# Kernel optimization log

Hardware: AMD Instinct MI355X
Metric: run time of the kernel (lower is better)

Reference implementation:

```python
import jax, jax.numpy as jnp
import numpy as np

EMBED_DIM = 768
N_HEADS = 12
HEAD_SIZE = EMBED_DIM // N_HEADS


def setup_inputs() -> dict:
    key = jax.random.key(0)
    k1, k2, k3, k4 = jax.random.split(key, 4)
    B, T, C = 512, 128, EMBED_DIM
    x = jax.random.normal(k1, (B, T, C), dtype=jnp.float32)
    # torch Linear weights: [out, in]
    w_qkv = jax.random.normal(k2, (3 * C, C), dtype=jnp.float32) / np.sqrt(C)
    w_proj = jax.random.normal(k3, (C, C), dtype=jnp.float32) / np.sqrt(C)
    b_proj = jax.random.normal(k4, (C,), dtype=jnp.float32) * 0.01
    return {"x": x, "w_qkv": w_qkv, "w_proj": w_proj, "b_proj": b_proj}


def reference(x, w_qkv, w_proj, b_proj):
    B, T, C = x.shape
    H, D = N_HEADS, HEAD_SIZE
    qkv = jnp.einsum('btc,oc->bto', x, w_qkv)  # [B,T,3C]
    q, k, v = jnp.split(qkv, 3, axis=-1)
    # [B,T,C] -> [B,H,T,D]
    q = q.reshape(B, T, H, D).transpose(0, 2, 1, 3)
    k = k.reshape(B, T, H, D).transpose(0, 2, 1, 3)
    v = v.reshape(B, T, H, D).transpose(0, 2, 1, 3)
    wei = jnp.einsum('bhtd,bhsd->bhts', q, k)  # [B,H,T,T]
    causal = jnp.tril(jnp.ones((T, T), dtype=bool))  # True where allowed
    wei = jnp.where(causal, wei, -jnp.inf)
    # original scales AFTER masking (-inf stays -inf)
    wei = jax.nn.softmax(wei / jnp.sqrt(jnp.asarray(D, x.dtype)), axis=-1)
    out = jnp.einsum('bhts,bhsd->bhtd', wei, v)  # [B,H,T,D]
    out = out.transpose(0, 2, 1, 3).reshape(B, T, C)
    # proj; dropout is identity in eval mode
    out = jnp.einsum('btc,oc->bto', out, w_proj) + b_proj
    return out
```

## Files before the change

### kernel.cpp

```cpp
#include <hip/hip_runtime.h>
#include <hip/hip_bf16.h>

typedef __bf16 bf16_t;
typedef __attribute__((ext_vector_type(8))) __bf16 bf16x8;
typedef __attribute__((ext_vector_type(4))) float f32x4;

#define B_SZ 512
#define T_SZ 128
#define C_SZ 768
#define H_SZ 12
#define D_SZ 64
#define M_SZ (B_SZ * T_SZ)
#define NQKV (3 * C_SZ)

__device__ __forceinline__ void cvt8(const float* in, bf16_t* out)
{
    float4 a = *reinterpret_cast<const float4*>(in);
    float4 b = *reinterpret_cast<const float4*>(in + 4);
    bf16x8 o;
    o[0] = (bf16_t)a.x; o[1] = (bf16_t)a.y;
    o[2] = (bf16_t)a.z; o[3] = (bf16_t)a.w;
    o[4] = (bf16_t)b.x; o[5] = (bf16_t)b.y;
    o[6] = (bf16_t)b.z; o[7] = (bf16_t)b.w;
    *reinterpret_cast<bf16x8*>(out) = o;
}

__global__ __launch_bounds__(256) void cvt3_f32_bf16(
    const float* __restrict__ x,  bf16_t* __restrict__ xb,
    const float* __restrict__ wq, bf16_t* __restrict__ wqb,
    const float* __restrict__ wp, bf16_t* __restrict__ wpb,
    int nx, int nq, int np)
{
    const int tot = (nx + nq + np) >> 3;
    int c = blockIdx.x * blockDim.x + threadIdx.x;
    const int stride = gridDim.x * blockDim.x;
    for (; c < tot; c += stride) {
        int i = c << 3;
        if (i < nx)            cvt8(x + i, xb + i);
        else if (i < nx + nq)  cvt8(wq + (i - nx), wqb + (i - nx));
        else                   cvt8(wp + (i - nx - nq), wpb + (i - nx - nq));
    }
}

__device__ __forceinline__ void gload16(const bf16_t* g, const char* l)
{
    __builtin_amdgcn_global_load_lds(
        (const __attribute__((address_space(1))) void*)g,
        (__attribute__((address_space(3))) void*)l, 16, 0, 0);
}

#define BAR() do { asm volatile("" ::: "memory"); \
                   __builtin_amdgcn_s_barrier(); \
                   asm volatile("" ::: "memory"); } while (0)

#define VMC(n) asm volatile("s_waitcnt vmcnt(" #n ")" ::: "memory")

#define LGKM0() do { asm volatile("s_waitcnt lgkmcnt(0)" ::: "memory"); \
                     __builtin_amdgcn_sched_barrier(0); } while (0)

#define RD_A0(bb) do { _Pragma("unroll") for (int m_ = 0; m_ < 4; ++m_) { \
    af0[m_][0] = *(const bf16x8*)(rdAk0 + (bb)*32768 + m_*2048); \
    af0[m_][1] = *(const bf16x8*)(rdAk1 + (bb)*32768 + m_*2048); } } while (0)

#define RD_AY(bb) do { _Pragma("unroll") for (int m_ = 0; m_ < 4; ++m_) { \
    afY[m_][0] = *(const bf16x8*)(rdAk0 + (bb)*32768 + 8192 + m_*2048); \
    afY[m_][1] = *(const bf16x8*)(rdAk1 + (bb)*32768 + 8192 + m_*2048); } } while (0)

#define RD_B01(bb) do { _Pragma("unroll") for (int n_ = 0; n_ < 2; ++n_) { \
    b01[n_][0] = *(const bf16x8*)(rdBk0 + (bb)*32768 + n_*2048); \
    b01[n_][1] = *(const bf16x8*)(rdBk1 + (bb)*32768 + n_*2048); } } while (0)

#define RD_B23(bb) do { _Pragma("unroll") for (int n_ = 0; n_ < 2; ++n_) { \
    b23[n_][0] = *(const bf16x8*)(rdBk0 + (bb)*32768 + 4096 + n_*2048); \
    b23[n_][1] = *(const bf16x8*)(rdBk1 + (bb)*32768 + 4096 + n_*2048); } } while (0)

#define ST_A(bb, hf, u) do { if ((u) < nt) { \
    const bf16_t* s_ = pA + (size_t)((hf)*128) * K + (size_t)(u)*64; \
    char* d_ = ldsAw + (bb)*32768 + (hf)*16384; \
    gload16(s_, d_); gload16(s_ + (size_t)8*K, d_ + 1024); } } while (0)

#define ST_B(bb, hf, u) do { if ((u) < nt) { \
    const bf16_t* s_ = pB + (size_t)((hf)*128) * K + (size_t)(u)*64; \
    char* d_ = ldsBw + (bb)*32768 + (hf)*16384; \
    gload16(s_, d_); gload16(s_ + (size_t)8*K, d_ + 1024); } } while (0)

#define MFQ(A_, B_, mo, no) do { \
    _Pragma("unroll") for (int m_ = 0; m_ < 4; ++m_) \
    _Pragma("unroll") for (int n_ = 0; n_ < 2; ++n_) { \
        acc[(mo)+m_][(no)+n_] = __builtin_amdgcn_mfma_f32_16x16x32_bf16( \
            A_[m_][0], B_[n_][0], acc[(mo)+m_][(no)+n_], 0, 0, 0); \
        acc[(mo)+m_][(no)+n_] = __builtin_amdgcn_mfma_f32_16x16x32_bf16( \
            A_[m_][1], B_[n_][1], acc[(mo)+m_][(no)+n_], 0, 0, 0); } \
    } while (0)

template <bool BF16_OUT, bool BIAS>
__global__ __launch_bounds__(512, 2) void gemm256(
    const bf16_t* __restrict__ A, const bf16_t* __restrict__ Bt,
    void* __restrict__ Cout, const float* __restrict__ bias,
    int M, int N, int K, int nx)
{
    __shared__ char smem[131072];

    const int tid  = threadIdx.x;
    const int lane = tid & 63;
    const int w    = tid >> 6;
    const int wr   = w >> 2;
    const int wc   = w & 3;

    const int nwg = gridDim.x;
    int bid = blockIdx.x;
    if ((nwg & 7) == 0) bid = (bid & 7) * (nwg >> 3) + (bid >> 3);
    const int bx = bid % nx;
    const int by = bid / nx;
    const size_t bm = (size_t)by * 256;
    const size_t bn = (size_t)bx * 256;

    const int nt    = K >> 6;
    const int niter = nt >> 1;

    const int i3    = lane >> 3;
    const int colSw = ((lane & 7) ^ i3) * 8;
    const bf16_t* pA = A  + (bm + (size_t)(w * 16 + i3)) * K + colSw;
    const bf16_t* pB = Bt + (bn + (size_t)(w * 16 + i3)) * K + colSw;
    char* ldsAw = smem + w * 2048;
    char* ldsBw = smem + 65536 + w * 2048;

    const int lane_lo = lane & 15;
    const int sxr  = (lane & 7) << 4;
    const int cK0  = (((lane >> 4) * 16) ^ sxr);
    const int cK1  = cK0 ^ 64;
    const char* rdAk0 = smem + wr * 16384 + lane_lo * 128 + cK0;
    const char* rdAk1 = smem + wr * 16384 + lane_lo * 128 + cK1;
    const char* rdBk0 = smem + 65536 + (wc >> 1) * 16384 + ((wc & 1) * 64 + lane_lo) * 128 + cK0;
    const char* rdBk1 = smem + 65536 + (wc >> 1) * 16384 + ((wc & 1) * 64 + lane_lo) * 128 + cK1;

    f32x4  acc[8][4] = {};
    bf16x8 af0[4][2], afY[4][2], b01[2][2], b23[2][2];

    ST_B(0, 0, 0); ST_A(0, 0, 0); ST_A(0, 1, 0); ST_B(0, 1, 0);
    ST_B(1, 0, 1); ST_A(1, 0, 1);
    VMC(4);
    BAR();

    for (int it = 0; it < niter; ++it) {
        const int u = it * 2;
        const bool last = (it + 1 == niter);
        RD_A0(0); RD_B01(0); RD_B23(0); ST_A(1, 1, u + 1); MFQ(af0, b01, 0, 0); BAR();
        RD_AY(0);                        ST_B(1, 1, u + 1); MFQ(af0, b23, 0, 2); BAR();
                                         ST_B(0, 0, u + 2); MFQ(afY, b01, 4, 0); BAR();
                                         ST_A(0, 0, u + 2); MFQ(afY, b23, 4, 2);
        if (last) { VMC(0); } else { VMC(4); }
        BAR();
        RD_A0(1); RD_B01(1); RD_B23(1); ST_A(0, 1, u + 2); MFQ(af0, b01, 0, 0); BAR();
        RD_AY(1);                        ST_B(0, 1, u + 2); MFQ(af0, b23, 0, 2); BAR();
                                         ST_B(1, 0, u + 3); MFQ(afY, b01, 4, 0); BAR();
                                         ST_A(1, 0, u + 3); MFQ(afY, b23, 4, 2);
        if (last) { VMC(0); } else { VMC(4); }
        BAR();
    }

    const int crow = (lane >> 4) * 4;
    const int ccol = lane & 15;
    if constexpr (BF16_OUT) {
        char* ep = smem + w * 16384;
        #pragma unroll
        for (int n = 0; n < 4; ++n) {
            const size_t col = bn + wc * 64 + n * 16 + ccol;
            float bv = 0.f;
            if constexpr (BIAS) bv = bias[col];
            #pragma unroll
            for (int m = 0; m < 8; ++m)
                #pragma unroll
                for (int r = 0; r < 4; ++r) {
                    const int rowloc = m * 16 + crow + r;
                    const int sw = ((rowloc & 7) << 4) ^ (((rowloc >> 3) & 1) << 5);
                    *(bf16_t*)(ep + rowloc * 128 + (((n * 16 + ccol) * 2) ^ sw))
                        = (bf16_t)(acc[m][n][r] + bv);
                }
        }
        LGKM0();
        bf16_t* cb = (bf16_t*)Cout;
        #pragma unroll
        for (int pass = 0; pass < 16; ++pass) {
            const int rloc = pass * 8 + (lane >> 3);
            const int ch   = lane & 7;
            const int sw   = ((rloc & 7) << 4) ^ (((rloc >> 3) & 1) << 5);
            bf16x8 v = *(const bf16x8*)(ep + rloc * 128 + ((ch * 16) ^ sw));
            *(bf16x8*)((char*)(cb + (bm + wr * 128 + rloc) * (size_t)N + bn + wc * 64) + ch * 16) = v;
        }
    } else {
        #pragma unroll
        for (int n = 0; n < 4; ++n) {
            const size_t col = bn + wc * 64 + n * 16 + ccol;
            float bv = 0.f;
            if constexpr (BIAS) bv = bias[col];
            #pragma unroll
            for (int m = 0; m < 8; ++m) {
                #pragma unroll
                for (int r = 0; r < 4; ++r) {
                    const size_t row = bm + wr * 128 + m * 16 + crow + r;
                    ((float*)Cout)[row * N + col] = acc[m][n][r] + bv;
                }
            }
        }
    }
}

__global__ __launch_bounds__(256) void attn_kernel(
    const bf16_t* __restrict__ qkv, bf16_t* __restrict__ outp)
{
    __shared__ bf16_t Ks[128 * 64];
    __shared__ bf16_t Vt[64 * 128];
    __shared__ bf16_t Ps[128 * 128];

    const int h    = blockIdx.x;
    const int b    = blockIdx.y;
    const int tid  = threadIdx.x;
    const int lane = tid & 63;
    const int wave = tid >> 6;

    const bf16_t* base = qkv + (size_t)b * T_SZ * NQKV + h * D_SZ;

    bf16x8 qf[2][2];
    #pragma unroll
    for (int mi = 0; mi < 2; ++mi)
        #pragma unroll
        for (int ks = 0; ks < 2; ++ks) {
            int m = wave * 32 + mi * 16 + (lane & 15);
            int d = ks * 32 + (lane >> 4) * 8;
            qf[mi][ks] = *reinterpret_cast<const bf16x8*>(base + (size_t)m * NQKV + d);
        }

    #pragma unroll
    for (int p = 0; p < 4; ++p) {
        int e   = p * 256 + tid;
        int row = e >> 3;
        int col = (e & 7) * 8;
        int4 kv = *reinterpret_cast<const int4*>(base + (size_t)row * NQKV + C_SZ + col);
        int kb = row * 128 + ((col * 2) ^ ((row & 7) << 4));
        *reinterpret_cast<int4*>((char*)Ks + kb) = kv;

        bf16x8 vv = *reinterpret_cast<const bf16x8*>(base + (size_t)row * NQKV + 2 * C_SZ + col);
        #pragma unroll
        for (int j = 0; j < 8; ++j) {
            int d  = col + j;
            int vb = d * 256 + ((row * 2) ^ ((d & 7) << 4));
            *reinterpret_cast<bf16_t*>((char*)Vt + vb) = vv[j];
        }
    }

    __syncthreads();

    f32x4 s[2][8] = {};
    #pragma unroll
    for (int ks = 0; ks < 2; ++ks) {
        int koff = ks * 32 + (lane >> 4) * 8;
        #pragma unroll
        for (int nj = 0; nj < 8; ++nj) {
            int n  = nj * 16 + (lane & 15);
            int kb = n * 128 + ((koff * 2) ^ ((n & 7) << 4));
            bf16x8 kf = *reinterpret_cast<const bf16x8*>((char*)Ks + kb);
            #pragma unroll
            for (int mi = 0; mi < 2; ++mi)
                s[mi][nj] = __builtin_amdgcn_mfma_f32_16x16x32_bf16(
                    qf[mi][ks], kf, s[mi][nj], 0, 0, 0);
        }
    }

    const float scale = 0.125f;
    #pragma unroll
    for (int mi = 0; mi < 2; ++mi) {
        #pragma unroll
        for (int r = 0; r < 4; ++r) {
            int m = wave * 32 + mi * 16 + ((lane >> 4) << 2) + r;
            float sv[8];
            float mx = -3.0e38f;
            #pragma unroll
            for (int nj = 0; nj < 8; ++nj) {
                int n   = nj * 16 + (lane & 15);
                float v = s[mi][nj][r] * scale;
                v = (n <= m) ? v : -3.0e38f;
                sv[nj] = v;
                mx = fmaxf(mx, v);
            }
            #pragma unroll
            for (int off = 1; off < 16; off <<= 1)
                mx = fmaxf(mx, __shfl_xor(mx, off));
            float sum = 0.f;
            #pragma unroll
            for (int nj = 0; nj < 8; ++nj) {
                float p = __expf(sv[nj] - mx);
                sv[nj] = p;
                sum += p;
            }
            #pragma unroll
            for (int off = 1; off < 16; off <<= 1)
                sum += __shfl_xor(sum, off);
            float inv = 1.0f / sum;
            #pragma unroll
            for (int nj = 0; nj < 8; ++nj) {
                int n  = nj * 16 + (lane & 15);
                int pb = m * 256 + ((n * 2) ^ ((m & 7) << 4));
                *reinterpret_cast<bf16_t*>((char*)Ps + pb) = (bf16_t)(sv[nj] * inv);
            }
        }
    }

    __syncthreads();

    f32x4 o[2][4] = {};
    #pragma unroll
    for (int ks = 0; ks < 4; ++ks) {
        int soff = ks * 32 + (lane >> 4) * 8;
        bf16x8 pf[2];
        #pragma unroll
        for (int mi = 0; mi < 2; ++mi) {
            int m  = wave * 32 + mi * 16 + (lane & 15);
            int pb = m * 256 + ((soff * 2) ^ ((m & 7) << 4));
            pf[mi] = *reinterpret_cast<const bf16x8*>((char*)Ps + pb);
        }
        #pragma unroll
        for (int nj = 0; nj < 4; ++nj) {
            int d  = nj * 16 + (lane & 15);
            int vb = d * 256 + ((soff * 2) ^ ((d & 7) << 4));
            bf16x8 vf = *reinterpret_cast<const bf16x8*>((char*)Vt + vb);
            #pragma unroll
            for (int mi = 0; mi < 2; ++mi)
                o[mi][nj] = __builtin_amdgcn_mfma_f32_16x16x32_bf16(
                    pf[mi], vf, o[mi][nj], 0, 0, 0);
        }
    }

    char* on = (char*)Ks;
    #pragma unroll
    for (int mi = 0; mi < 2; ++mi)
        #pragma unroll
        for (int nj = 0; nj < 4; ++nj)
            #pragma unroll
            for (int r = 0; r < 4; ++r) {
                int m = wave * 32 + mi * 16 + ((lane >> 4) << 2) + r;
                int d = nj * 16 + (lane & 15);
                *(bf16_t*)(on + m * 128 + d * 2) = (bf16_t)o[mi][nj][r];
            }

    __syncthreads();

    bf16_t* op = outp + (size_t)b * T_SZ * C_SZ + h * D_SZ;
    #pragma unroll
    for (int pass = 0; pass < 4; ++pass) {
        int row = pass * 32 + (tid >> 3);
        int ch  = tid & 7;
        bf16x8 v = *(const bf16x8*)(on + row * 128 + ch * 16);
        *(bf16x8*)((char*)(op + (size_t)row * C_SZ) + ch * 16) = v;
    }
}

extern "C" void kernel_launch(void* const* d_in, const int* in_sizes, int n_in,
                              void* d_out, int out_size, void* d_ws, size_t ws_size,
                              hipStream_t stream)
{
    const float* x      = (const float*)d_in[0];
    const float* w_qkv  = (const float*)d_in[1];
    const float* w_proj = (const float*)d_in[2];
    const float* b_proj = (const float*)d_in[3];

    const int n_x     = M_SZ * C_SZ;
    const int n_wqkv  = NQKV * C_SZ;
    const int n_wproj = C_SZ * C_SZ;

    char* ws = (char*)d_ws;
    bf16_t* xb     = (bf16_t*)ws;
    bf16_t* wqkvb  = (bf16_t*)(ws + (size_t)n_x * 2);
    bf16_t* wprojb = (bf16_t*)(ws + (size_t)n_x * 2 + (size_t)n_wqkv * 2);
    bf16_t* qkvb   = (bf16_t*)(ws + (size_t)n_x * 2 + (size_t)n_wqkv * 2 + (size_t)n_wproj * 2);
    bf16_t* attnb  = xb;

    cvt3_f32_bf16<<<4096, 256, 0, stream>>>(x, xb, w_qkv, wqkvb, w_proj, wprojb,
                                            n_x, n_wqkv, n_wproj);

    gemm256<true, false><<<dim3((NQKV / 256) * (M_SZ / 256)), 512, 0, stream>>>(
        xb, wqkvb, qkvb, nullptr, M_SZ, NQKV, C_SZ, NQKV / 256);

    attn_kernel<<<dim3(H_SZ, B_SZ), 256, 0, stream>>>(qkvb, attnb);

    gemm256<false, true><<<dim3((C_SZ / 256) * (M_SZ / 256)), 512, 0, stream>>>(
        attnb, wprojb, d_out, b_proj, M_SZ, C_SZ, C_SZ, C_SZ / 256);
}
```

Measured before the change: 509.8 us.

## Replace QKV GEMM with 128x128 K32 double-buffered bf16 MFMA kernel

Adds a new GEMM kernel using 128x128 output tiles with K-step 32, four waves each owning a 64x64 sub-tile, and two LDS stages filled by direct global-to-LDS loads with a swizzled layout. The epilogue stages bf16 results through LDS for coalesced 16-byte stores. The QKV projection now uses this kernel in place of the 256x256 tile kernel, aiming for higher occupancy (up to 4 blocks per CU) and more blocks across the GPU. The trade-off is lower data reuse per tile and a barrier every 32-wide K step.

```diff
diff --git a/kernel.cpp b/kernel.cpp
--- a/kernel.cpp
+++ b/kernel.cpp
@@ -57,6 +57,107 @@
 
 #define LGKM0() do { asm volatile("s_waitcnt lgkmcnt(0)" ::: "memory"); \
                      __builtin_amdgcn_sched_barrier(0); } while (0)
+
+#define K32_ST_A(bb, u) do { if ((u) < nt) { \
+    const bf16_t* s_ = pA + (size_t)(u) * 32; \
+    char* d_ = ldsAw + (bb)*8192; \
+    gload16(s_, d_); gload16(s_ + (size_t)16*K, d_ + 1024); } } while (0)
+
+#define K32_ST_B(bb, u) do { if ((u) < nt) { \
+    const bf16_t* s_ = pB + (size_t)(u) * 32; \
+    char* d_ = ldsBw + (bb)*8192; \
+    gload16(s_, d_); gload16(s_ + (size_t)16*K, d_ + 1024); } } while (0)
+
+#define K32_RD(bb) do { _Pragma("unroll") for (int m_ = 0; m_ < 4; ++m_) { \
+    af[m_] = *(const bf16x8*)(rdA + (bb)*8192 + m_*1024); \
+    bfr[m_] = *(const bf16x8*)(rdB + (bb)*8192 + m_*1024); } } while (0)
+
+#define K32_MFALL() do { \
+    _Pragma("unroll") for (int m_ = 0; m_ < 4; ++m_) \
+    _Pragma("unroll") for (int n_ = 0; n_ < 4; ++n_) \
+        acc[m_][n_] = __builtin_amdgcn_mfma_f32_16x16x32_bf16( \
+            af[m_], bfr[n_], acc[m_][n_], 0, 0, 0); \
+    } while (0)
+
+__global__ __launch_bounds__(256, 4) void gemm128k32(
+    const bf16_t* __restrict__ A, const bf16_t* __restrict__ Bt,
+    bf16_t* __restrict__ Cout, int M, int N, int K, int nx)
+{
+    __shared__ char smem[32768];
+
+    const int tid  = threadIdx.x;
+    const int lane = tid & 63;
+    const int w    = tid >> 6;
+    const int wr   = w >> 1;
+    const int wc   = w & 1;
+
+    const int nwg = gridDim.x;
+    int bid = blockIdx.x;
+    if ((nwg & 7) == 0) bid = (bid & 7) * (nwg >> 3) + (bid >> 3);
+    const int bx = bid % nx;
+    const int by = bid / nx;
+    const size_t bm = (size_t)by * 128;
+    const size_t bn = (size_t)bx * 128;
+
+    const int nt = K >> 5;
+
+    const int i2 = lane >> 2;
+    const int c4 = lane & 3;
+    const int cSw = (c4 ^ ((i2 >> 1) & 3)) * 8;
+    const bf16_t* pA = A  + (bm + (size_t)(w * 32 + i2)) * K + cSw;
+    const bf16_t* pB = Bt + (bn + (size_t)(w * 32 + i2)) * K + cSw;
+    char* ldsAw = smem + w * 2048;
+    char* ldsBw = smem + 16384 + w * 2048;
+
+    const int lane_lo = lane & 15;
+    const int cK = ((lane >> 4) << 4) ^ (((lane_lo >> 1) & 3) << 4);
+    const char* rdA = smem + (wr * 64 + lane_lo) * 64 + cK;
+    const char* rdB = smem + 16384 + (wc * 64 + lane_lo) * 64 + cK;
+
+    f32x4  acc[4][4] = {};
+    bf16x8 af[4], bfr[4];
+
+    K32_ST_A(0, 0); K32_ST_B(0, 0);
+    VMC(0);
+    BAR();
+
+    for (int it = 0; it < nt / 2; ++it) {
+        const int u = it * 2;
+        K32_ST_A(1, u + 1); K32_ST_B(1, u + 1);
+        K32_RD(0);
+        K32_MFALL();
+        VMC(0); BAR();
+        K32_ST_A(0, u + 2); K32_ST_B(0, u + 2);
+        K32_RD(1);
+        K32_MFALL();
+        VMC(0); BAR();
+    }
+
+    const int crow = (lane >> 4) * 4;
+    const int ccol = lane & 15;
+    char* ep = smem + w * 8192;
+    #pragma unroll
+    for (int n = 0; n < 4; ++n) {
+        #pragma unroll
+        for (int m = 0; m < 4; ++m)
+            #pragma unroll
+            for (int r = 0; r < 4; ++r) {
+                const int rowloc = m * 16 + crow + r;
+                const int sw = ((rowloc & 7) << 4) ^ (((rowloc >> 3) & 1) << 5);
+                *(bf16_t*)(ep + rowloc * 128 + (((n * 16 + ccol) * 2) ^ sw))
+                    = (bf16_t)acc[m][n][r];
+            }
+    }
+    LGKM0();
+    #pragma unroll
+    for (int pass = 0; pass < 8; ++pass) {
+        const int rloc = pass * 8 + (lane >> 3);
+        const int ch   = lane & 7;
+        const int sw   = ((rloc & 7) << 4) ^ (((rloc >> 3) & 1) << 5);
+        bf16x8 v = *(const bf16x8*)(ep + rloc * 128 + ((ch * 16) ^ sw));
+        *(bf16x8*)((char*)(Cout + (bm + wr * 64 + rloc) * (size_t)N + bn + wc * 64) + ch * 16) = v;
+    }
+}
 
 #define RD_A0(bb) do { _Pragma("unroll") for (int m_ = 0; m_ < 4; ++m_) { \
     af0[m_][0] = *(const bf16x8*)(rdAk0 + (bb)*32768 + m_*2048); \
@@ -378,8 +479,8 @@
     cvt3_f32_bf16<<<4096, 256, 0, stream>>>(x, xb, w_qkv, wqkvb, w_proj, wprojb,
                                             n_x, n_wqkv, n_wproj);
 
-    gemm256<true, false><<<dim3((NQKV / 256) * (M_SZ / 256)), 512, 0, stream>>>(
-        xb, wqkvb, qkvb, nullptr, M_SZ, NQKV, C_SZ, NQKV / 256);
+    gemm128k32<<<dim3((NQKV / 128) * (M_SZ / 128)), 256, 0, stream>>>(
+        xb, wqkvb, qkvb, M_SZ, NQKV, C_SZ, NQKV / 128);
 
     attn_kernel<<<dim3(H_SZ, B_SZ), 256, 0, stream>>>(qkvb, attnb);
 
```

Measured after the change: 561.8 us. 1.1x slower.
